# Performance work log

Measured on AMD Instinct MI355X. Metric: run time of the kernel, lower is better.

The kernel has to match this reference:

```python
import jax, jax.numpy as jnp
import numpy as np


def setup_inputs() -> dict:
    key = jax.random.key(0)
    k1, k2, k3, k4, k5, k6 = jax.random.split(key, 6)
    N, M = 4096, 4096      # data matrix
    K, D = 2048, 1024      # parameter matrix K x K, similarity matrix K x D
    Npair = 128            # size of i/j index subsets
    return {
        "actual": jax.random.normal(k1, (N, M), dtype=jnp.float32),
        "prediction": jax.random.normal(k2, (N, M), dtype=jnp.float32),
        "lamb": jnp.asarray(0.1, dtype=jnp.float32),
        "P": jax.random.normal(k3, (K, K), dtype=jnp.float32),
        "S": jax.random.normal(k4, (K, D), dtype=jnp.float32),
        "i_indices": jax.random.randint(k5, (Npair,), 0, K, dtype=jnp.int64),
        "j_indices": jax.random.randint(k6, (Npair,), 0, K, dtype=jnp.int64),
    }


def _safe_norm_rows(diff):
    # L2 norm over last axis with a zero-safe sqrt (grad is 0 at exactly-0 diffs,
    # matching torch's subgradient convention for .norm()).
    d2 = jnp.sum(diff * diff, axis=-1)
    pos = d2 > 0
    return jnp.sqrt(jnp.where(pos, d2, 1.0)) * pos


def reference(actual, prediction, lamb, P, S, i_indices, j_indices):
    # (p > 0) * clamp(p, min=0) == relu(p)
    Pp = jnp.maximum(P, 0.0)
    # penalty term: ||relu(P)||_F
    penalty = jnp.linalg.norm(Pp)
    # pairwise parameter-similarity penalty:
    # sum_{i in I, j in J} relu(P)[i,j] * || S[i,:] - S[j,:] ||_2
    Si = S[i_indices]                       # [Ni, D]
    Sj = S[j_indices]                       # [Nj, D]
    diff = Si[:, None, :] - Sj[None, :, :]  # [Ni, Nj, D]
    norms = _safe_norm_rows(diff)           # [Ni, Nj]
    Pij = Pp[i_indices[:, None], j_indices[None, :]]  # [Ni, Nj]
    parameter_penalty = jnp.sum(Pij * norms)
    data_term = jnp.linalg.norm(actual - prediction)
    return data_term + lamb * (penalty + parameter_penalty)
```

## Files before the change

### kernel.cpp

```cpp
#include <hip/hip_runtime.h>
#include <math.h>

#define BR 1024
#define BP 1024
#define TPB 256

__device__ __forceinline__ float waveReduceSum(float v) {
    #pragma unroll
    for (int off = 32; off > 0; off >>= 1)
        v += __shfl_down(v, off, 64);
    return v;
}

__global__ __launch_bounds__(256, 8)
void fused_kernel(const float* __restrict__ a,
                  const float* __restrict__ p,
                  const float* __restrict__ Pm,
                  const float* __restrict__ S,
                  const int* __restrict__ ii,
                  const int* __restrict__ jj,
                  float* __restrict__ ws,
                  long nAP, long nP, int Npair, int D, int K)
{
    __shared__ float sm0[4], sm1[4];
    const int wave = threadIdx.x >> 6;
    const int lane = threadIdx.x & 63;
    const int bid  = blockIdx.x;

    if (bid < BP) {
        const int totalPairs = Npair * Npair;
        const int base = bid * 16 + wave * 4;
        float local = 0.f;

        if (base < totalPairs && D == 1024 && (base % Npair) + 3 < Npair) {
            const int i  = base / Npair;
            const int j0 = base - i * Npair;
            const int ri = ii[i];
            const float4* Si4 = (const float4*)(S + (long)ri * D);
            float4 x0 = Si4[lane];
            float4 x1 = Si4[lane + 64];
            float4 x2 = Si4[lane + 128];
            float4 x3 = Si4[lane + 192];
            const long riK = (long)ri * K;

            float d2q[4];
            int   rjq[4];
            #pragma unroll
            for (int q = 0; q < 4; ++q) {
                const int rj = jj[j0 + q];
                rjq[q] = rj;
                const float4* Sj4 = (const float4*)(S + (long)rj * D);
                float4 y0 = Sj4[lane];
                float4 y1 = Sj4[lane + 64];
                float4 y2 = Sj4[lane + 128];
                float4 y3 = Sj4[lane + 192];
                float d2 = 0.f, e;
                e = x0.x - y0.x; d2 += e * e;
                e = x0.y - y0.y; d2 += e * e;
                e = x0.z - y0.z; d2 += e * e;
                e = x0.w - y0.w; d2 += e * e;
                e = x1.x - y1.x; d2 += e * e;
                e = x1.y - y1.y; d2 += e * e;
                e = x1.z - y1.z; d2 += e * e;
                e = x1.w - y1.w; d2 += e * e;
                e = x2.x - y2.x; d2 += e * e;
                e = x2.y - y2.y; d2 += e * e;
                e = x2.z - y2.z; d2 += e * e;
                e = x2.w - y2.w; d2 += e * e;
                e = x3.x - y3.x; d2 += e * e;
                e = x3.y - y3.y; d2 += e * e;
                e = x3.z - y3.z; d2 += e * e;
                e = x3.w - y3.w; d2 += e * e;
                d2q[q] = d2;
            }
            #pragma unroll
            for (int q = 0; q < 4; ++q)
                d2q[q] = waveReduceSum(d2q[q]);
            if (lane == 0) {
                #pragma unroll
                for (int q = 0; q < 4; ++q)
                    if (d2q[q] > 0.f)
                        local += fmaxf(Pm[riK + rjq[q]], 0.f) * sqrtf(d2q[q]);
            }
        } else {
            #pragma unroll
            for (int q = 0; q < 4; ++q) {
                int pair = base + q;
                if (pair < totalPairs) {
                    int i = pair / Npair;
                    int j = pair - i * Npair;
                    int ri = ii[i];
                    int rj = jj[j];
                    const float* Si = S + (long)ri * D;
                    const float* Sj = S + (long)rj * D;
                    float d2 = 0.f;
                    for (int c = lane; c < D; c += 64) {
                        float e = Si[c] - Sj[c];
                        d2 += e * e;
                    }
                    d2 = waveReduceSum(d2);
                    if (lane == 0 && d2 > 0.f)
                        local += fmaxf(Pm[(long)ri * K + rj], 0.f) * sqrtf(d2);
                }
            }
        }
        if (lane == 0) sm0[wave] = local;
        __syncthreads();
        if (threadIdx.x == 0)
            ws[2 * BR + bid] = sm0[0] + sm0[1] + sm0[2] + sm0[3];
    } else {
        const int rb = bid - BP;
        const long tid    = (long)rb * TPB + threadIdx.x;
        const long stride = (long)BR * TPB;

        const float4* a4 = (const float4*)a;
        const float4* p4 = (const float4*)p;
        long n4 = nAP >> 2;

        float s0a = 0.f, s0b = 0.f, s0c = 0.f, s0d = 0.f;
        long i = tid;
        for (; i + 3 * stride < n4; i += 4 * stride) {
            float4 av0 = a4[i];
            float4 av1 = a4[i + stride];
            float4 av2 = a4[i + 2 * stride];
            float4 av3 = a4[i + 3 * stride];
            float4 pv0 = p4[i];
            float4 pv1 = p4[i + stride];
            float4 pv2 = p4[i + 2 * stride];
            float4 pv3 = p4[i + 3 * stride];
            __builtin_amdgcn_sched_barrier(0);
            float d;
            d = av0.x - pv0.x; s0a += d * d;
            d = av0.y - pv0.y; s0a += d * d;
            d = av0.z - pv0.z; s0a += d * d;
            d = av0.w - pv0.w; s0a += d * d;
            d = av1.x - pv1.x; s0b += d * d;
            d = av1.y - pv1.y; s0b += d * d;
            d = av1.z - pv1.z; s0b += d * d;
            d = av1.w - pv1.w; s0b += d * d;
            d = av2.x - pv2.x; s0c += d * d;
            d = av2.y - pv2.y; s0c += d * d;
            d = av2.z - pv2.z; s0c += d * d;
            d = av2.w - pv2.w; s0c += d * d;
            d = av3.x - pv3.x; s0d += d * d;
            d = av3.y - pv3.y; s0d += d * d;
            d = av3.z - pv3.z; s0d += d * d;
            d = av3.w - pv3.w; s0d += d * d;
        }
        for (; i < n4; i += stride) {
            float4 av = a4[i], pv = p4[i];
            float d;
            d = av.x - pv.x; s0a += d * d;
            d = av.y - pv.y; s0a += d * d;
            d = av.z - pv.z; s0a += d * d;
            d = av.w - pv.w; s0a += d * d;
        }

        const float4* P4 = (const float4*)Pm;
        long nP4 = nP >> 2;
        float s1a = 0.f, s1b = 0.f;
        i = tid;
        for (; i + stride < nP4; i += 2 * stride) {
            float4 v0 = P4[i];
            float4 v1 = P4[i + stride];
            __builtin_amdgcn_sched_barrier(0);
            float r;
            r = fmaxf(v0.x, 0.f); s1a += r * r;
            r = fmaxf(v0.y, 0.f); s1a += r * r;
            r = fmaxf(v0.z, 0.f); s1a += r * r;
            r = fmaxf(v0.w, 0.f); s1a += r * r;
            r = fmaxf(v1.x, 0.f); s1b += r * r;
            r = fmaxf(v1.y, 0.f); s1b += r * r;
            r = fmaxf(v1.z, 0.f); s1b += r * r;
            r = fmaxf(v1.w, 0.f); s1b += r * r;
        }
        for (; i < nP4; i += stride) {
            float4 v = P4[i];
            float r;
            r = fmaxf(v.x, 0.f); s1a += r * r;
            r = fmaxf(v.y, 0.f); s1a += r * r;
            r = fmaxf(v.z, 0.f); s1a += r * r;
            r = fmaxf(v.w, 0.f); s1a += r * r;
        }

        float s0 = waveReduceSum(s0a + s0b + s0c + s0d);
        float s1 = waveReduceSum(s1a + s1b);
        if (lane == 0) { sm0[wave] = s0; sm1[wave] = s1; }
        __syncthreads();
        if (threadIdx.x == 0) {
            ws[rb]      = sm0[0] + sm0[1] + sm0[2] + sm0[3];
            ws[BR + rb] = sm1[0] + sm1[1] + sm1[2] + sm1[3];
        }
    }
}

__global__ void finalize_kernel(const float* __restrict__ ws,
                                const float* __restrict__ lamb,
                                float* __restrict__ out)
{
    float a0 = 0.f, a1 = 0.f, a2 = 0.f;
    for (int i = threadIdx.x; i < BR; i += TPB) {
        a0 += ws[i];
        a1 += ws[BR + i];
    }
    for (int i = threadIdx.x; i < BP; i += TPB)
        a2 += ws[2 * BR + i];

    a0 = waveReduceSum(a0);
    a1 = waveReduceSum(a1);
    a2 = waveReduceSum(a2);

    __shared__ float m0[4], m1[4], m2[4];
    int wave = threadIdx.x >> 6;
    int lane = threadIdx.x & 63;
    if (lane == 0) { m0[wave] = a0; m1[wave] = a1; m2[wave] = a2; }
    __syncthreads();
    if (threadIdx.x == 0) {
        float A0 = m0[0] + m0[1] + m0[2] + m0[3];
        float A1 = m1[0] + m1[1] + m1[2] + m1[3];
        float A2 = m2[0] + m2[1] + m2[2] + m2[3];
        out[0] = sqrtf(A0) + lamb[0] * (sqrtf(A1) + A2);
    }
}

extern "C" void kernel_launch(void* const* d_in, const int* in_sizes, int n_in,
                              void* d_out, int out_size, void* d_ws, size_t ws_size,
                              hipStream_t stream) {
    const float* actual = (const float*)d_in[0];
    const float* pred   = (const float*)d_in[1];
    const float* lamb   = (const float*)d_in[2];
    const float* Pm     = (const float*)d_in[3];
    const float* S      = (const float*)d_in[4];
    const int*   ii     = (const int*)d_in[5];
    const int*   jj     = (const int*)d_in[6];
    float* out = (float*)d_out;
    float* ws  = (float*)d_ws;

    long nAP   = in_sizes[0];
    long nP    = in_sizes[3];
    int  K     = (int)lround(sqrt((double)nP));
    int  Npair = in_sizes[5];
    int  D     = (int)(in_sizes[4] / K);

    fused_kernel<<<BP + BR, TPB, 0, stream>>>(actual, pred, Pm, S, ii, jj, ws,
                                              nAP, nP, Npair, D, K);
    finalize_kernel<<<1, TPB, 0, stream>>>(ws, lamb, out);
}
```

Before: 35.79 us.

## Halve block counts and software-pipeline streaming loads with double buffering

Cuts both the pair-penalty and reduction block counts from 1024 to 512. Each pair wave now handles 8 pairs instead of 4, reusing the loaded Si row across more Sj rows. The data-term loop becomes a fully unrolled, double-buffered pipeline that issues the next batch of loads before consuming the current one, and the P norm loads all its values up front. This is meant to keep more memory requests in flight per thread and to reduce per-block overhead, at the cost of higher register pressure (launch bounds relaxed to 4 blocks) and fast paths tied to exact sizes.

```diff
diff --git a/kernel.cpp b/kernel.cpp
--- a/kernel.cpp
+++ b/kernel.cpp
@@ -1,8 +1,8 @@
 #include <hip/hip_runtime.h>
 #include <math.h>
 
-#define BR 1024
-#define BP 1024
+#define PBN 512
+#define RBN 512
 #define TPB 256
 
 __device__ __forceinline__ float waveReduceSum(float v) {
@@ -12,7 +12,19 @@
     return v;
 }
 
-__global__ __launch_bounds__(256, 8)
+#define CONS(AV, PV, S) { float d_;                       \
+    d_ = (AV).x - (PV).x; S += d_ * d_;                   \
+    d_ = (AV).y - (PV).y; S += d_ * d_;                   \
+    d_ = (AV).z - (PV).z; S += d_ * d_;                   \
+    d_ = (AV).w - (PV).w; S += d_ * d_; }
+
+#define RCONS(V, S) { float r_;                           \
+    r_ = fmaxf((V).x, 0.f); S += r_ * r_;                 \
+    r_ = fmaxf((V).y, 0.f); S += r_ * r_;                 \
+    r_ = fmaxf((V).z, 0.f); S += r_ * r_;                 \
+    r_ = fmaxf((V).w, 0.f); S += r_ * r_; }
+
+__global__ __launch_bounds__(TPB, 4)
 void fused_kernel(const float* __restrict__ a,
                   const float* __restrict__ p,
                   const float* __restrict__ Pm,
@@ -27,15 +39,15 @@
     const int lane = threadIdx.x & 63;
     const int bid  = blockIdx.x;
 
-    if (bid < BP) {
+    if (bid < PBN) {
         const int totalPairs = Npair * Npair;
-        const int base = bid * 16 + wave * 4;
+        const int base = bid * 32 + wave * 8;
         float local = 0.f;
 
-        if (base < totalPairs && D == 1024 && (base % Npair) + 3 < Npair) {
-            const int i  = base / Npair;
-            const int j0 = base - i * Npair;
-            const int ri = ii[i];
+        if (D == 1024 && base + 7 < totalPairs && (base % Npair) + 7 < Npair) {
+            const int ig = base / Npair;
+            const int j0 = base - ig * Npair;
+            const int ri = ii[ig];
             const float4* Si4 = (const float4*)(S + (long)ri * D);
             float4 x0 = Si4[lane];
             float4 x1 = Si4[lane + 64];
@@ -43,10 +55,10 @@
             float4 x3 = Si4[lane + 192];
             const long riK = (long)ri * K;
 
-            float d2q[4];
-            int   rjq[4];
-            #pragma unroll
-            for (int q = 0; q < 4; ++q) {
+            float d2q[8];
+            int   rjq[8];
+            #pragma unroll
+            for (int q = 0; q < 8; ++q) {
                 const int rj = jj[j0 + q];
                 rjq[q] = rj;
                 const float4* Sj4 = (const float4*)(S + (long)rj * D);
@@ -74,22 +86,21 @@
                 d2q[q] = d2;
             }
             #pragma unroll
-            for (int q = 0; q < 4; ++q)
+            for (int q = 0; q < 8; ++q)
                 d2q[q] = waveReduceSum(d2q[q]);
             if (lane == 0) {
                 #pragma unroll
-                for (int q = 0; q < 4; ++q)
+                for (int q = 0; q < 8; ++q)
                     if (d2q[q] > 0.f)
                         local += fmaxf(Pm[riK + rjq[q]], 0.f) * sqrtf(d2q[q]);
             }
         } else {
-            #pragma unroll
-            for (int q = 0; q < 4; ++q) {
+            for (int q = 0; q < 8; ++q) {
                 int pair = base + q;
                 if (pair < totalPairs) {
-                    int i = pair / Npair;
-                    int j = pair - i * Npair;
-                    int ri = ii[i];
+                    int ig = pair / Npair;
+                    int j  = pair - ig * Npair;
+                    int ri = ii[ig];
                     int rj = jj[j];
                     const float* Si = S + (long)ri * D;
                     const float* Sj = S + (long)rj * D;
@@ -107,80 +118,75 @@
         if (lane == 0) sm0[wave] = local;
         __syncthreads();
         if (threadIdx.x == 0)
-            ws[2 * BR + bid] = sm0[0] + sm0[1] + sm0[2] + sm0[3];
+            ws[2 * RBN + bid] = sm0[0] + sm0[1] + sm0[2] + sm0[3];
     } else {
-        const int rb = bid - BP;
+        const int  rb     = bid - PBN;
         const long tid    = (long)rb * TPB + threadIdx.x;
-        const long stride = (long)BR * TPB;
+        const long stride = (long)RBN * TPB;
 
         const float4* a4 = (const float4*)a;
         const float4* p4 = (const float4*)p;
-        long n4 = nAP >> 2;
+        const long n4  = nAP >> 2;
+        const long nP4 = nP  >> 2;
 
         float s0a = 0.f, s0b = 0.f, s0c = 0.f, s0d = 0.f;
-        long i = tid;
-        for (; i + 3 * stride < n4; i += 4 * stride) {
-            float4 av0 = a4[i];
-            float4 av1 = a4[i + stride];
-            float4 av2 = a4[i + 2 * stride];
-            float4 av3 = a4[i + 3 * stride];
-            float4 pv0 = p4[i];
-            float4 pv1 = p4[i + stride];
-            float4 pv2 = p4[i + 2 * stride];
-            float4 pv3 = p4[i + 3 * stride];
+
+        if (n4 == 32L * stride) {
+            float4 A[2][4], Pv[2][4];
+            long i = tid;
+            #pragma unroll
+            for (int u = 0; u < 4; ++u) {
+                A[0][u]  = a4[i + u * stride];
+                Pv[0][u] = p4[i + u * stride];
+            }
+            i += 4 * stride;
+            #pragma unroll
+            for (int it = 1; it < 8; ++it) {
+                const int nxt = it & 1;
+                const int cur = nxt ^ 1;
+                #pragma unroll
+                for (int u = 0; u < 4; ++u) {
+                    A[nxt][u]  = a4[i + u * stride];
+                    Pv[nxt][u] = p4[i + u * stride];
+                }
+                i += 4 * stride;
+                __builtin_amdgcn_sched_barrier(0);
+                CONS(A[cur][0], Pv[cur][0], s0a);
+                CONS(A[cur][1], Pv[cur][1], s0b);
+                CONS(A[cur][2], Pv[cur][2], s0c);
+                CONS(A[cur][3], Pv[cur][3], s0d);
+            }
+            CONS(A[1][0], Pv[1][0], s0a);
+            CONS(A[1][1], Pv[1][1], s0b);
+            CONS(A[1][2], Pv[1][2], s0c);
+            CONS(A[1][3], Pv[1][3], s0d);
+        } else {
+            for (long i = tid; i < n4; i += stride) {
+                float4 av = a4[i], pv = p4[i];
+                CONS(av, pv, s0a);
+            }
+        }
+
+        const float4* P4 = (const float4*)Pm;
+        float s1a = 0.f, s1b = 0.f;
+        if (nP4 == 8L * stride) {
+            float4 B[2][4];
+            long q = tid;
+            #pragma unroll
+            for (int u = 0; u < 4; ++u) B[0][u] = P4[q + u * stride];
+            q += 4 * stride;
+            #pragma unroll
+            for (int u = 0; u < 4; ++u) B[1][u] = P4[q + u * stride];
             __builtin_amdgcn_sched_barrier(0);
-            float d;
-            d = av0.x - pv0.x; s0a += d * d;
-            d = av0.y - pv0.y; s0a += d * d;
-            d = av0.z - pv0.z; s0a += d * d;
-            d = av0.w - pv0.w; s0a += d * d;
-            d = av1.x - pv1.x; s0b += d * d;
-            d = av1.y - pv1.y; s0b += d * d;
-            d = av1.z - pv1.z; s0b += d * d;
-            d = av1.w - pv1.w; s0b += d * d;
-            d = av2.x - pv2.x; s0c += d * d;
-            d = av2.y - pv2.y; s0c += d * d;
-            d = av2.z - pv2.z; s0c += d * d;
-            d = av2.w - pv2.w; s0c += d * d;
-            d = av3.x - pv3.x; s0d += d * d;
-            d = av3.y - pv3.y; s0d += d * d;
-            d = av3.z - pv3.z; s0d += d * d;
-            d = av3.w - pv3.w; s0d += d * d;
-        }
-        for (; i < n4; i += stride) {
-            float4 av = a4[i], pv = p4[i];
-            float d;
-            d = av.x - pv.x; s0a += d * d;
-            d = av.y - pv.y; s0a += d * d;
-            d = av.z - pv.z; s0a += d * d;
-            d = av.w - pv.w; s0a += d * d;
-        }
-
-        const float4* P4 = (const float4*)Pm;
-        long nP4 = nP >> 2;
-        float s1a = 0.f, s1b = 0.f;
-        i = tid;
-        for (; i + stride < nP4; i += 2 * stride) {
-            float4 v0 = P4[i];
-            float4 v1 = P4[i + stride];
-            __builtin_amdgcn_sched_barrier(0);
-            float r;
-            r = fmaxf(v0.x, 0.f); s1a += r * r;
-            r = fmaxf(v0.y, 0.f); s1a += r * r;
-            r = fmaxf(v0.z, 0.f); s1a += r * r;
-            r = fmaxf(v0.w, 0.f); s1a += r * r;
-            r = fmaxf(v1.x, 0.f); s1b += r * r;
-            r = fmaxf(v1.y, 0.f); s1b += r * r;
-            r = fmaxf(v1.z, 0.f); s1b += r * r;
-            r = fmaxf(v1.w, 0.f); s1b += r * r;
-        }
-        for (; i < nP4; i += stride) {
-            float4 v = P4[i];
-            float r;
-            r = fmaxf(v.x, 0.f); s1a += r * r;
-            r = fmaxf(v.y, 0.f); s1a += r * r;
-            r = fmaxf(v.z, 0.f); s1a += r * r;
-            r = fmaxf(v.w, 0.f); s1a += r * r;
+            RCONS(B[0][0], s1a); RCONS(B[0][1], s1b);
+            RCONS(B[0][2], s1a); RCONS(B[0][3], s1b);
+            RCONS(B[1][0], s1a); RCONS(B[1][1], s1b);
+            RCONS(B[1][2], s1a); RCONS(B[1][3], s1b);
+        } else {
+            for (long q = tid; q < nP4; q += stride) {
+                float4 v = P4[q];
+                RCONS(v, s1a);
+            }
         }
 
         float s0 = waveReduceSum(s0a + s0b + s0c + s0d);
@@ -188,8 +194,8 @@
         if (lane == 0) { sm0[wave] = s0; sm1[wave] = s1; }
         __syncthreads();
         if (threadIdx.x == 0) {
-            ws[rb]      = sm0[0] + sm0[1] + sm0[2] + sm0[3];
-            ws[BR + rb] = sm1[0] + sm1[1] + sm1[2] + sm1[3];
+            ws[rb]       = sm0[0] + sm0[1] + sm0[2] + sm0[3];
+            ws[RBN + rb] = sm1[0] + sm1[1] + sm1[2] + sm1[3];
         }
     }
 }
@@ -199,12 +205,12 @@
                                 float* __restrict__ out)
 {
     float a0 = 0.f, a1 = 0.f, a2 = 0.f;
-    for (int i = threadIdx.x; i < BR; i += TPB) {
+    for (int i = threadIdx.x; i < RBN; i += TPB) {
         a0 += ws[i];
-        a1 += ws[BR + i];
+        a1 += ws[RBN + i];
     }
-    for (int i = threadIdx.x; i < BP; i += TPB)
-        a2 += ws[2 * BR + i];
+    for (int i = threadIdx.x; i < PBN; i += TPB)
+        a2 += ws[2 * RBN + i];
 
     a0 = waveReduceSum(a0);
     a1 = waveReduceSum(a1);
@@ -242,7 +248,7 @@
     int  Npair = in_sizes[5];
     int  D     = (int)(in_sizes[4] / K);
 
-    fused_kernel<<<BP + BR, TPB, 0, stream>>>(actual, pred, Pm, S, ii, jj, ws,
-                                              nAP, nP, Npair, D, K);
+    fused_kernel<<<PBN + RBN, TPB, 0, stream>>>(actual, pred, Pm, S, ii, jj, ws,
+                                                nAP, nP, Npair, D, K);
     finalize_kernel<<<1, TPB, 0, stream>>>(ws, lamb, out);
 }
```

Measured after the change: 32.49 us. -9.2%, faster.
